# Kernel tuning notes

Measured on AMD Instinct MI355X. Metric: run time of the kernel, lower is better.

The kernel has to match this reference:

```python
import jax, jax.numpy as jnp
import numpy as np

B = 16384
N_NARR = 128
N_SUB = 1024
K = N_SUB // N_NARR  # narrative i -> subnarratives [i*K, (i+1)*K)
GAMMA = 2.0
NW, SW, HW = 1.0, 1.0, 0.5  # narrative/subnarrative/hierarchy weights


def setup_inputs() -> dict:
    key = jax.random.key(0)
    k1, k2, k3, k4 = jax.random.split(key, 4)
    return {
        "narrative_logits": jax.random.normal(k1, (B, N_NARR), jnp.float32),
        "subnarrative_logits": jax.random.normal(k2, (B, N_SUB), jnp.float32),
        "narrative_labels": jax.random.randint(k3, (B, N_NARR), 0, 2, jnp.int32),
        "subnarrative_labels": jax.random.randint(k4, (B, N_SUB), 0, 2, jnp.int32),
    }


def _weighted_bce(logits, labels, pos_weight):
    # BCEWithLogits with pos_weight: pw*y*softplus(-x) + (1-y)*softplus(x)
    return pos_weight * labels * jax.nn.softplus(-logits) + (1.0 - labels) * jax.nn.softplus(logits)


def reference(narrative_logits, subnarrative_logits, narrative_labels, subnarrative_labels):
    nl = narrative_labels.astype(jnp.float32)
    sl = subnarrative_labels.astype(jnp.float32)
    b = narrative_logits.shape[0]

    # class-balanced pos_weights, clamped to [1, 50]
    npw = jnp.clip((1.0 - nl).sum(0) / (nl.sum(0) + 1e-6), 1.0, 50.0)
    spw = jnp.clip((1.0 - sl).sum(0) / (sl.sum(0) + 1e-6), 1.0, 50.0)

    narrative_loss = _weighted_bce(narrative_logits, nl, npw).mean()

    # ragged subnarrative loss, vectorized: groups of K subnarrs per narrative.
    # per-(sample, positive-narrative) mean BCE over the group, averaged over
    # the number of valid (sample, narrative) pairs -- same math as the loop.
    sub_bce = _weighted_bce(subnarrative_logits, sl, spw).reshape(b, N_NARR, K)
    per_group = sub_bce.mean(-1)              # [B, N_NARR]
    pos = nl                                   # positive-narrative mask [B, N_NARR]
    valid_count = pos.sum()
    subnarrative_loss = jnp.where(
        valid_count > 0, (per_group * pos).sum() / jnp.maximum(valid_count, 1.0), 0.0)

    # hierarchy consistency: relu(max subnarr prob - narr prob) over positives
    nprob = jax.nn.sigmoid(narrative_logits)
    sprob = jax.nn.sigmoid(subnarrative_logits)
    grp_max = sprob.reshape(b, N_NARR, K).max(-1)  # [B, N_NARR]
    hierarchy_loss = (jax.nn.relu(grp_max - nprob) * pos).sum() / b

    # focal terms (mean over all elements)
    nf = ((1.0 - nprob) ** GAMMA * nl * jax.nn.log_sigmoid(narrative_logits)).mean()
    sf = ((1.0 - sprob) ** GAMMA * sl * jax.nn.log_sigmoid(subnarrative_logits)).mean()

    total = (NW * (narrative_loss - 0.1 * nf)
             + SW * (subnarrative_loss - 0.1 * sf)
             + HW * hierarchy_loss)
    return total
```

## Files before the change

kernel.cpp:

```cpp
#include <hip/hip_runtime.h>


#define BDIM 256
#define NROWS 16384
#define NNARR 128
#define NSUB 1024

#define NSLICES 8
#define SUBC 128
#define NARRC 16
#define ROWS_PER_CHUNK 64
#define NCHUNKS (NROWS / ROWS_PER_CHUNK)
#define NBLOCKS (NCHUNKS * NSLICES)
#define ROWS_PER_PASS 8
#define ITERS (ROWS_PER_CHUNK / ROWS_PER_PASS)

#define PE_NARR 384
#define PE_SC   432
#define PUSED   435
#define PSTRIDE 448

#define NGRP 8
#define CHUNKS_PER_GRP (NCHUNKS / NGRP)
#define TSTRIDE 448

__device__ __forceinline__ void bce_pieces(float x, float& sp_p, float& sp_m, float& sig) {
    float a = fabsf(x);
    float e = __expf(-a);
    float l = __logf(1.0f + e);
    sp_p = fmaxf(x, 0.0f) + l;
    sp_m = sp_p - x;
    float inv = __builtin_amdgcn_rcpf(1.0f + e);
    sig = (x >= 0.0f) ? inv : e * inv;
}

__global__ __launch_bounds__(BDIM, 4) void ncl_main(
    const float* __restrict__ nlog, const float* __restrict__ slog,
    const int*   __restrict__ nlab, const int*   __restrict__ slab,
    float* __restrict__ P)
{
    __shared__ float lsub[4][32][12];
    __shared__ float lnar[4][16][3];
    __shared__ float lsc[4][3];

    const int t     = threadIdx.x;
    const int j     = blockIdx.x & (NSLICES - 1);
    const int chunk = blockIdx.x >> 3;
    const int q  = t & 31;
    const int ro = t >> 5;
    const int cl = q >> 1;
    const bool evenq = (q & 1) == 0;

    const int r0 = chunk * ROWS_PER_CHUNK + ro;
    const float* sp = slog + (size_t)r0 * NSUB  + j * SUBC  + 4 * q;
    const int*   yp = slab + (size_t)r0 * NSUB  + j * SUBC  + 4 * q;
    const float* np = nlog + (size_t)r0 * NNARR + j * NARRC + cl;
    const int*   mp = nlab + (size_t)r0 * NNARR + j * NARRC + cl;

    float As[4] = {0,0,0,0}, Cs[4] = {0,0,0,0}, ssum[4] = {0,0,0,0};
    float An = 0.f, Cn = 0.f, ns = 0.f, fn = 0.f, fs = 0.f, hier = 0.f;

    float4 xs = *(const float4*)sp;
    int4   ys = *(const int4*)  yp;
    float  nx   = *np;
    float  posv = (float)*mp;

    #pragma unroll
    for (int it = 0; it < ITERS; ++it) {
        float4 xs_n; int4 ys_n; float nx_n = 0.f, posv_n = 0.f;
        if (it + 1 < ITERS) {
            const size_t so = (size_t)(it + 1) * ROWS_PER_PASS * NSUB;
            const size_t no = (size_t)(it + 1) * ROWS_PER_PASS * NNARR;
            xs_n   = *(const float4*)(sp + so);
            ys_n   = *(const int4*)  (yp + so);
            nx_n   = np[no];
            posv_n = (float)mp[no];
        }

        float nsp_p, nsp_m, nsig;
        bce_pieces(nx, nsp_p, nsp_m, nsig);

        const float xv[4] = {xs.x, xs.y, xs.z, xs.w};
        const float yv[4] = {(float)ys.x, (float)ys.y, (float)ys.z, (float)ys.w};
        float mymax = 0.0f;
        #pragma unroll
        for (int k = 0; k < 4; ++k) {
            float sp_p, sp_m, sig;
            bce_pieces(xv[k], sp_p, sp_m, sig);
            float y = yv[k];
            As[k]   += posv * y * sp_m;
            Cs[k]   += posv * (1.0f - y) * sp_p;
            ssum[k] += y;
            float om = 1.0f - sig;
            fs += om * om * y * (-sp_m);
            mymax = fmaxf(mymax, sig);
        }
        float gmax = fmaxf(mymax, __shfl_xor(mymax, 1, 64));
        if (evenq) {
            hier += fmaxf(gmax - nsig, 0.0f) * posv;
            An += posv * nsp_m;
            Cn += (1.0f - posv) * nsp_p;
            ns += posv;
            float om = 1.0f - nsig;
            fn += om * om * posv * (-nsp_m);
        }

        if (it + 1 < ITERS) { xs = xs_n; ys = ys_n; nx = nx_n; posv = posv_n; }
    }

    #pragma unroll
    for (int k = 0; k < 4; ++k) {
        As[k]   += __shfl_xor(As[k],   32, 64);
        Cs[k]   += __shfl_xor(Cs[k],   32, 64);
        ssum[k] += __shfl_xor(ssum[k], 32, 64);
    }
    An += __shfl_xor(An, 32, 64);
    Cn += __shfl_xor(Cn, 32, 64);
    ns += __shfl_xor(ns, 32, 64);
    #pragma unroll
    for (int m = 1; m <= 32; m <<= 1) {
        fn   += __shfl_xor(fn,   m, 64);
        fs   += __shfl_xor(fs,   m, 64);
        hier += __shfl_xor(hier, m, 64);
    }

    const int w = t >> 6, lane = t & 63;
    if (lane < 32) {
        #pragma unroll
        for (int k = 0; k < 4; ++k) {
            lsub[w][lane][k]     = As[k];
            lsub[w][lane][4 + k] = Cs[k];
            lsub[w][lane][8 + k] = ssum[k];
        }
        if ((lane & 1) == 0) {
            lnar[w][lane >> 1][0] = An;
            lnar[w][lane >> 1][1] = Cn;
            lnar[w][lane >> 1][2] = ns;
        }
    }
    if (lane == 0) { lsc[w][0] = fn; lsc[w][1] = fs; lsc[w][2] = hier; }
    __syncthreads();

    float* const Pb = P + (size_t)blockIdx.x * PSTRIDE;
    if (t < 32) {
        float a[12];
        #pragma unroll
        for (int k = 0; k < 12; ++k)
            a[k] = lsub[0][t][k] + lsub[1][t][k] + lsub[2][t][k] + lsub[3][t][k];
        *(float4*)(Pb + t * 12 + 0) = make_float4(a[0], a[1], a[2],  a[3]);
        *(float4*)(Pb + t * 12 + 4) = make_float4(a[4], a[5], a[6],  a[7]);
        *(float4*)(Pb + t * 12 + 8) = make_float4(a[8], a[9], a[10], a[11]);
    } else if (t < 48) {
        const int c = t - 32;
        Pb[PE_NARR + c * 3 + 0] = lnar[0][c][0] + lnar[1][c][0] + lnar[2][c][0] + lnar[3][c][0];
        Pb[PE_NARR + c * 3 + 1] = lnar[0][c][1] + lnar[1][c][1] + lnar[2][c][1] + lnar[3][c][1];
        Pb[PE_NARR + c * 3 + 2] = lnar[0][c][2] + lnar[1][c][2] + lnar[2][c][2] + lnar[3][c][2];
    } else if (t == 48) {
        Pb[PE_SC + 0] = lsc[0][0] + lsc[1][0] + lsc[2][0] + lsc[3][0];
        Pb[PE_SC + 1] = lsc[0][1] + lsc[1][1] + lsc[2][1] + lsc[3][1];
        Pb[PE_SC + 2] = lsc[0][2] + lsc[1][2] + lsc[2][2] + lsc[3][2];
    }
}

__global__ __launch_bounds__(256) void ncl_sreduce(const float* __restrict__ P,
                                                   float* __restrict__ tmp)
{
    const int g = blockIdx.x;
    const int j = blockIdx.y;
    const int t = threadIdx.x;
    const bool hi = t < (PSTRIDE - 256);

    float s0 = 0.f, s1 = 0.f;
    #pragma unroll 4
    for (int cc = 0; cc < CHUNKS_PER_GRP; ++cc) {
        const int c = g * CHUNKS_PER_GRP + cc;
        const float* p = P + (size_t)(c * NSLICES + j) * PSTRIDE;
        s0 += p[t];
        if (hi) s1 += p[t + 256];
    }
    float* o = tmp + (size_t)(g * NSLICES + j) * TSTRIDE;
    o[t] = s0;
    if (hi) o[t + 256] = s1;
}

__global__ __launch_bounds__(1024) void ncl_finalize(const float* __restrict__ tmp,
                                                     float* __restrict__ out)
{
    __shared__ float sr[6][16];
    const int t = threadIdx.x;
    const float Bf = (float)NROWS;

    {
    }
    const int j  = t >> 7;
    const int cs = t & 127;
    const int q  = cs >> 2;
    const int k  = cs & 3;
    float As = 0.f, Csv = 0.f, ss = 0.f;
    #pragma unroll
    for (int g = 0; g < NGRP; ++g) {
        const float* p = tmp + (size_t)(g * NSLICES + j) * TSTRIDE + q * 12 + k;
        As  += p[0];
        Csv += p[4];
        ss  += p[8];
    }
    float spw = fminf(fmaxf((Bf - ss) / (ss + 1e-6f), 1.0f), 50.0f);
    float sub_part = spw * As + Csv;

    float narr_part = 0.f, valid_part = 0.f;
    if (t < NNARR) {
        const int jn = t >> 4, c = t & 15;
        float An = 0.f, Cn = 0.f, ns = 0.f;
        #pragma unroll
        for (int g = 0; g < NGRP; ++g) {
            const float* p = tmp + (size_t)(g * NSLICES + jn) * TSTRIDE + PE_NARR + c * 3;
            An += p[0]; Cn += p[1]; ns += p[2];
        }
        float npw = fminf(fmaxf((Bf - ns) / (ns + 1e-6f), 1.0f), 50.0f);
        narr_part  = npw * An + Cn;
        valid_part = ns;
    }

    float fn_p = 0.f, fs_p = 0.f, hier_p = 0.f;
    if (t < NGRP * NSLICES) {
        const float* p = tmp + (size_t)t * TSTRIDE + PE_SC;
        fn_p = p[0]; fs_p = p[1]; hier_p = p[2];
    }

    #pragma unroll
    for (int off = 32; off; off >>= 1) {
        sub_part   += __shfl_down(sub_part,   off, 64);
        narr_part  += __shfl_down(narr_part,  off, 64);
        valid_part += __shfl_down(valid_part, off, 64);
        fn_p       += __shfl_down(fn_p,       off, 64);
        fs_p       += __shfl_down(fs_p,       off, 64);
        hier_p     += __shfl_down(hier_p,     off, 64);
    }
    if ((t & 63) == 0) {
        int w = t >> 6;
        sr[0][w] = sub_part; sr[1][w] = narr_part; sr[2][w] = valid_part;
        sr[3][w] = fn_p;     sr[4][w] = fs_p;      sr[5][w] = hier_p;
    }
    __syncthreads();
    if (t == 0) {
        float sub_tot = 0.f, narr_tot = 0.f, valid = 0.f;
        float fn = 0.f, fs = 0.f, hier = 0.f;
        #pragma unroll
        for (int i = 0; i < 16; ++i) {
            sub_tot += sr[0][i]; narr_tot += sr[1][i]; valid += sr[2][i];
            fn += sr[3][i]; fs += sr[4][i]; hier += sr[5][i];
        }

        float narrative_loss = narr_tot / (Bf * (float)NNARR);
        float sub_loss = (valid > 0.0f) ? (sub_tot * (1.0f / 8.0f)) / fmaxf(valid, 1.0f) : 0.0f;
        float nf = fn / (Bf * (float)NNARR);
        float sf = fs / (Bf * (float)NSUB);
        float hier_loss = hier / Bf;

        out[0] = (narrative_loss - 0.1f * nf)
               + (sub_loss       - 0.1f * sf)
               + 0.5f * hier_loss;
    }
}

extern "C" void kernel_launch(void* const* d_in, const int* in_sizes, int n_in,
                              void* d_out, int out_size, void* d_ws, size_t ws_size,
                              hipStream_t stream) {
    const float* nlog = (const float*)d_in[0];
    const float* slog = (const float*)d_in[1];
    const int*   nlab = (const int*)d_in[2];
    const int*   slab = (const int*)d_in[3];
    float* P   = (float*)d_ws;
    float* tmp = P + (size_t)NBLOCKS * PSTRIDE;
    float* out = (float*)d_out;

    ncl_main<<<NBLOCKS, BDIM, 0, stream>>>(nlog, slog, nlab, slab, P);
    dim3 gr(NGRP, NSLICES);
    ncl_sreduce<<<gr, 256, 0, stream>>>(P, tmp);
    ncl_finalize<<<1, 1024, 0, stream>>>(tmp, out);
}
```

Baseline: 206.6 us.

## Give each block full rows instead of column slices, reshape partial reduction

The main kernel stops splitting each row into eight column slices. Each 512-thread block now covers 16 full rows, two rows per pass with 256 threads per row. Per-column partials are combined through shared memory between the two row halves, and the second-stage reduction becomes a flat per-element sum over groups of blocks. The intent is to make each block read contiguous full rows and to simplify the partial layout. The cost is a much larger partial buffer per block (about 3.4K floats across 1024 blocks), which raises traffic in the reduction stage, and the explicit software prefetch of the next rows is dropped.

```diff
diff --git a/kernel.cpp b/kernel.cpp
--- a/kernel.cpp
+++ b/kernel.cpp
@@ -1,28 +1,23 @@
 #include <hip/hip_runtime.h>
 
 
-#define BDIM 256
+#define BDIM 512
 #define NROWS 16384
 #define NNARR 128
 #define NSUB 1024
 
-#define NSLICES 8
-#define SUBC 128
-#define NARRC 16
-#define ROWS_PER_CHUNK 64
-#define NCHUNKS (NROWS / ROWS_PER_CHUNK)
-#define NBLOCKS (NCHUNKS * NSLICES)
-#define ROWS_PER_PASS 8
-#define ITERS (ROWS_PER_CHUNK / ROWS_PER_PASS)
-
-#define PE_NARR 384
-#define PE_SC   432
-#define PUSED   435
-#define PSTRIDE 448
-
-#define NGRP 8
-#define CHUNKS_PER_GRP (NCHUNKS / NGRP)
-#define TSTRIDE 448
+#define ROWS_PER_BLOCK 16
+#define NBLOCKS (NROWS / ROWS_PER_BLOCK)
+#define ITERS (ROWS_PER_BLOCK / 2)
+
+#define PSUB   0
+#define PNARR  3072
+#define PSC    3456
+#define PUSED  3459
+#define PSTRIDE 3472
+
+#define NGRP 16
+#define TPG (NBLOCKS / NGRP)
 
 __device__ __forceinline__ void bce_pieces(float x, float& sp_p, float& sp_m, float& sig) {
     float a = fabsf(x);
@@ -34,48 +29,38 @@
     sig = (x >= 0.0f) ? inv : e * inv;
 }
 
-__global__ __launch_bounds__(BDIM, 4) void ncl_main(
+__global__ __launch_bounds__(BDIM, 8) void ncl_main(
     const float* __restrict__ nlog, const float* __restrict__ slog,
     const int*   __restrict__ nlab, const int*   __restrict__ slab,
     float* __restrict__ P)
 {
-    __shared__ float lsub[4][32][12];
-    __shared__ float lnar[4][16][3];
-    __shared__ float lsc[4][3];
-
-    const int t     = threadIdx.x;
-    const int j     = blockIdx.x & (NSLICES - 1);
-    const int chunk = blockIdx.x >> 3;
-    const int q  = t & 31;
-    const int ro = t >> 5;
-    const int cl = q >> 1;
-    const bool evenq = (q & 1) == 0;
-
-    const int r0 = chunk * ROWS_PER_CHUNK + ro;
-    const float* sp = slog + (size_t)r0 * NSUB  + j * SUBC  + 4 * q;
-    const int*   yp = slab + (size_t)r0 * NSUB  + j * SUBC  + 4 * q;
-    const float* np = nlog + (size_t)r0 * NNARR + j * NARRC + cl;
-    const int*   mp = nlab + (size_t)r0 * NNARR + j * NARRC + cl;
+    __shared__ float lsub[256][12];
+    __shared__ float lnar[128][3];
+    __shared__ float lsc[8][3];
+
+    const int t  = threadIdx.x;
+    const int tc = t & 255;
+    const int rs = t >> 8;
+    const int nc = tc >> 1;
+    const bool even = (tc & 1) == 0;
+
+    const int r0 = blockIdx.x * ROWS_PER_BLOCK + rs;
+    const float* sp = slog + (size_t)r0 * NSUB  + 4 * tc;
+    const int*   yp = slab + (size_t)r0 * NSUB  + 4 * tc;
+    const float* np = nlog + (size_t)r0 * NNARR + nc;
+    const int*   mp = nlab + (size_t)r0 * NNARR + nc;
 
     float As[4] = {0,0,0,0}, Cs[4] = {0,0,0,0}, ssum[4] = {0,0,0,0};
     float An = 0.f, Cn = 0.f, ns = 0.f, fn = 0.f, fs = 0.f, hier = 0.f;
 
-    float4 xs = *(const float4*)sp;
-    int4   ys = *(const int4*)  yp;
-    float  nx   = *np;
-    float  posv = (float)*mp;
-
-    #pragma unroll
-    for (int it = 0; it < ITERS; ++it) {
-        float4 xs_n; int4 ys_n; float nx_n = 0.f, posv_n = 0.f;
-        if (it + 1 < ITERS) {
-            const size_t so = (size_t)(it + 1) * ROWS_PER_PASS * NSUB;
-            const size_t no = (size_t)(it + 1) * ROWS_PER_PASS * NNARR;
-            xs_n   = *(const float4*)(sp + so);
-            ys_n   = *(const int4*)  (yp + so);
-            nx_n   = np[no];
-            posv_n = (float)mp[no];
-        }
+    #pragma unroll 4
+    for (int i = 0; i < ITERS; ++i) {
+        const size_t so = (size_t)(2 * i) * NSUB;
+        const size_t no = (size_t)(2 * i) * NNARR;
+        const float4 xs = *(const float4*)(sp + so);
+        const int4   ys = *(const int4*)  (yp + so);
+        const float  nx   = np[no];
+        const float  posv = (float)mp[no];
 
         float nsp_p, nsp_m, nsig;
         bce_pieces(nx, nsp_p, nsp_m, nsig);
@@ -96,7 +81,7 @@
             mymax = fmaxf(mymax, sig);
         }
         float gmax = fmaxf(mymax, __shfl_xor(mymax, 1, 64));
-        if (evenq) {
+        if (even) {
             hier += fmaxf(gmax - nsig, 0.0f) * posv;
             An += posv * nsp_m;
             Cn += (1.0f - posv) * nsp_p;
@@ -104,83 +89,67 @@
             float om = 1.0f - nsig;
             fn += om * om * posv * (-nsp_m);
         }
-
-        if (it + 1 < ITERS) { xs = xs_n; ys = ys_n; nx = nx_n; posv = posv_n; }
-    }
-
-    #pragma unroll
-    for (int k = 0; k < 4; ++k) {
-        As[k]   += __shfl_xor(As[k],   32, 64);
-        Cs[k]   += __shfl_xor(Cs[k],   32, 64);
-        ssum[k] += __shfl_xor(ssum[k], 32, 64);
-    }
-    An += __shfl_xor(An, 32, 64);
-    Cn += __shfl_xor(Cn, 32, 64);
-    ns += __shfl_xor(ns, 32, 64);
+    }
+
     #pragma unroll
     for (int m = 1; m <= 32; m <<= 1) {
         fn   += __shfl_xor(fn,   m, 64);
         fs   += __shfl_xor(fs,   m, 64);
         hier += __shfl_xor(hier, m, 64);
     }
-
-    const int w = t >> 6, lane = t & 63;
-    if (lane < 32) {
+    if ((t & 63) == 0) {
+        const int w = t >> 6;
+        lsc[w][0] = fn; lsc[w][1] = fs; lsc[w][2] = hier;
+    }
+
+    if (rs == 1) {
         #pragma unroll
         for (int k = 0; k < 4; ++k) {
-            lsub[w][lane][k]     = As[k];
-            lsub[w][lane][4 + k] = Cs[k];
-            lsub[w][lane][8 + k] = ssum[k];
-        }
-        if ((lane & 1) == 0) {
-            lnar[w][lane >> 1][0] = An;
-            lnar[w][lane >> 1][1] = Cn;
-            lnar[w][lane >> 1][2] = ns;
-        }
-    }
-    if (lane == 0) { lsc[w][0] = fn; lsc[w][1] = fs; lsc[w][2] = hier; }
+            lsub[tc][k]     = As[k];
+            lsub[tc][4 + k] = Cs[k];
+            lsub[tc][8 + k] = ssum[k];
+        }
+        if (even) { lnar[nc][0] = An; lnar[nc][1] = Cn; lnar[nc][2] = ns; }
+    }
     __syncthreads();
 
     float* const Pb = P + (size_t)blockIdx.x * PSTRIDE;
-    if (t < 32) {
+    if (rs == 0) {
         float a[12];
         #pragma unroll
-        for (int k = 0; k < 12; ++k)
-            a[k] = lsub[0][t][k] + lsub[1][t][k] + lsub[2][t][k] + lsub[3][t][k];
-        *(float4*)(Pb + t * 12 + 0) = make_float4(a[0], a[1], a[2],  a[3]);
-        *(float4*)(Pb + t * 12 + 4) = make_float4(a[4], a[5], a[6],  a[7]);
-        *(float4*)(Pb + t * 12 + 8) = make_float4(a[8], a[9], a[10], a[11]);
-    } else if (t < 48) {
-        const int c = t - 32;
-        Pb[PE_NARR + c * 3 + 0] = lnar[0][c][0] + lnar[1][c][0] + lnar[2][c][0] + lnar[3][c][0];
-        Pb[PE_NARR + c * 3 + 1] = lnar[0][c][1] + lnar[1][c][1] + lnar[2][c][1] + lnar[3][c][1];
-        Pb[PE_NARR + c * 3 + 2] = lnar[0][c][2] + lnar[1][c][2] + lnar[2][c][2] + lnar[3][c][2];
-    } else if (t == 48) {
-        Pb[PE_SC + 0] = lsc[0][0] + lsc[1][0] + lsc[2][0] + lsc[3][0];
-        Pb[PE_SC + 1] = lsc[0][1] + lsc[1][1] + lsc[2][1] + lsc[3][1];
-        Pb[PE_SC + 2] = lsc[0][2] + lsc[1][2] + lsc[2][2] + lsc[3][2];
-    }
-}
-
-__global__ __launch_bounds__(256) void ncl_sreduce(const float* __restrict__ P,
+        for (int k = 0; k < 4; ++k) {
+            a[k]     = As[k]   + lsub[tc][k];
+            a[4 + k] = Cs[k]   + lsub[tc][4 + k];
+            a[8 + k] = ssum[k] + lsub[tc][8 + k];
+        }
+        *(float4*)(Pb + PSUB + tc * 12 + 0) = make_float4(a[0], a[1], a[2],  a[3]);
+        *(float4*)(Pb + PSUB + tc * 12 + 4) = make_float4(a[4], a[5], a[6],  a[7]);
+        *(float4*)(Pb + PSUB + tc * 12 + 8) = make_float4(a[8], a[9], a[10], a[11]);
+        if (even) {
+            Pb[PNARR + nc * 3 + 0] = An + lnar[nc][0];
+            Pb[PNARR + nc * 3 + 1] = Cn + lnar[nc][1];
+            Pb[PNARR + nc * 3 + 2] = ns + lnar[nc][2];
+        }
+    }
+    if (t == 0) {
+        float a = 0.f, b = 0.f, c = 0.f;
+        #pragma unroll
+        for (int w = 0; w < 8; ++w) { a += lsc[w][0]; b += lsc[w][1]; c += lsc[w][2]; }
+        Pb[PSC + 0] = a; Pb[PSC + 1] = b; Pb[PSC + 2] = c;
+    }
+}
+
+__global__ __launch_bounds__(256) void ncl_reduce1(const float* __restrict__ P,
                                                    float* __restrict__ tmp)
 {
-    const int g = blockIdx.x;
-    const int j = blockIdx.y;
-    const int t = threadIdx.x;
-    const bool hi = t < (PSTRIDE - 256);
-
-    float s0 = 0.f, s1 = 0.f;
+    const int e = blockIdx.x * 256 + threadIdx.x;
+    if (e >= PUSED) return;
+    const int g = blockIdx.y;
+    float s = 0.f;
     #pragma unroll 4
-    for (int cc = 0; cc < CHUNKS_PER_GRP; ++cc) {
-        const int c = g * CHUNKS_PER_GRP + cc;
-        const float* p = P + (size_t)(c * NSLICES + j) * PSTRIDE;
-        s0 += p[t];
-        if (hi) s1 += p[t + 256];
-    }
-    float* o = tmp + (size_t)(g * NSLICES + j) * TSTRIDE;
-    o[t] = s0;
-    if (hi) o[t + 256] = s1;
+    for (int i = 0; i < TPG; ++i)
+        s += P[(size_t)(g * TPG + i) * PSTRIDE + e];
+    tmp[(size_t)g * PSTRIDE + e] = s;
 }
 
 __global__ __launch_bounds__(1024) void ncl_finalize(const float* __restrict__ tmp,
@@ -190,16 +159,11 @@
     const int t = threadIdx.x;
     const float Bf = (float)NROWS;
 
-    {
-    }
-    const int j  = t >> 7;
-    const int cs = t & 127;
-    const int q  = cs >> 2;
-    const int k  = cs & 3;
+    const int q = t >> 2, k = t & 3;
     float As = 0.f, Csv = 0.f, ss = 0.f;
     #pragma unroll
     for (int g = 0; g < NGRP; ++g) {
-        const float* p = tmp + (size_t)(g * NSLICES + j) * TSTRIDE + q * 12 + k;
+        const float* p = tmp + (size_t)g * PSTRIDE + PSUB + q * 12 + k;
         As  += p[0];
         Csv += p[4];
         ss  += p[8];
@@ -209,11 +173,10 @@
 
     float narr_part = 0.f, valid_part = 0.f;
     if (t < NNARR) {
-        const int jn = t >> 4, c = t & 15;
         float An = 0.f, Cn = 0.f, ns = 0.f;
         #pragma unroll
         for (int g = 0; g < NGRP; ++g) {
-            const float* p = tmp + (size_t)(g * NSLICES + jn) * TSTRIDE + PE_NARR + c * 3;
+            const float* p = tmp + (size_t)g * PSTRIDE + PNARR + t * 3;
             An += p[0]; Cn += p[1]; ns += p[2];
         }
         float npw = fminf(fmaxf((Bf - ns) / (ns + 1e-6f), 1.0f), 50.0f);
@@ -222,8 +185,8 @@
     }
 
     float fn_p = 0.f, fs_p = 0.f, hier_p = 0.f;
-    if (t < NGRP * NSLICES) {
-        const float* p = tmp + (size_t)t * TSTRIDE + PE_SC;
+    if (t < NGRP) {
+        const float* p = tmp + (size_t)t * PSTRIDE + PSC;
         fn_p = p[0]; fs_p = p[1]; hier_p = p[2];
     }
 
@@ -275,7 +238,7 @@
     float* out = (float*)d_out;
 
     ncl_main<<<NBLOCKS, BDIM, 0, stream>>>(nlog, slog, nlab, slab, P);
-    dim3 gr(NGRP, NSLICES);
-    ncl_sreduce<<<gr, 256, 0, stream>>>(P, tmp);
+    dim3 gr((PUSED + 255) / 256, NGRP);
+    ncl_reduce1<<<gr, 256, 0, stream>>>(P, tmp);
     ncl_finalize<<<1, 1024, 0, stream>>>(tmp, out);
 }
```

Result: slower. 257.0 us (+24.4%).
